# Optimization experiments

Measured on AMD Instinct MI355X. Metric: run time of the kernel, lower is better.

Reference implementation:

```python
import jax, jax.numpy as jnp
import numpy as np
import math

EMBED_DIM = 1024
NUM_HEADS = 16
HEAD_DIM = EMBED_DIM // NUM_HEADS  # 64
MAX_SEQ_LEN = 2048


def rope_tables(max_seq_len, dim):
    pos = jnp.arange(max_seq_len, dtype=jnp.float32)
    div_term = jnp.exp(jnp.arange(0, dim, 2, dtype=jnp.float32) * -(math.log(10000.0) / dim))
    ang = pos[:, None] * div_term[None, :]  # [S, dim//2]
    return jnp.sin(ang), jnp.cos(ang)


def apply_rope(x, sin, cos):
    # x: [B, H, S, D]; sin/cos: [max_seq, D//2]
    S = x.shape[2]
    sin = sin[:S][None, None]  # [1,1,S,D//2]
    cos = cos[:S][None, None]
    x1, x2 = jnp.split(x, 2, axis=-1)
    return jnp.concatenate([cos * x1 - sin * x2, sin * x1 + cos * x2], axis=-1)


def setup_inputs() -> dict:
    key = jax.random.key(0)
    ks = jax.random.split(key, 5)
    B, S, E = 4, 2048, EMBED_DIM
    std = 1.0 / math.sqrt(E)
    x = jax.random.normal(ks[0], (B, S, E), dtype=jnp.float32)
    Wq = jax.random.normal(ks[1], (E, E), dtype=jnp.float32) * std
    Wk = jax.random.normal(ks[2], (E, E), dtype=jnp.float32) * std
    Wv = jax.random.normal(ks[3], (E, E), dtype=jnp.float32) * std
    Wo = jax.random.normal(ks[4], (E, E), dtype=jnp.float32) * std
    return {"x": x, "Wq": Wq, "Wk": Wk, "Wv": Wv, "Wo": Wo}


def reference(x, Wq, Wk, Wv, Wo):
    B, S, E = x.shape
    H, D = NUM_HEADS, HEAD_DIM
    scale = 1.0 / math.sqrt(D)
    sin, cos = rope_tables(MAX_SEQ_LEN, D)

    def split_heads(t):
        return t.reshape(B, S, H, D).transpose(0, 2, 1, 3)  # [B,H,S,D]

    q = split_heads(x @ Wq)
    k = split_heads(x @ Wk)
    v = split_heads(x @ Wv)
    q = apply_rope(q, sin, cos)
    k = apply_rope(k, sin, cos)

    scores = jnp.einsum('bhqd,bhkd->bhqk', q, k) * scale
    causal = jnp.where(jnp.tril(jnp.ones((S, S), dtype=bool)), 0.0, -1e9)
    scores = scores + causal[None, None]
    attn = jax.nn.softmax(scores, axis=-1)
    out = jnp.einsum('bhqk,bhkd->bhqd', attn, v)  # [B,H,S,D]
    out = out.transpose(0, 2, 1, 3).reshape(B, S, E)
    return out @ Wo
```

## Files before the change

kernel.cpp:

```cpp
#include <hip/hip_runtime.h>

#define DEVFN __device__ __forceinline__

typedef __attribute__((ext_vector_type(8))) short bf16x8;
typedef __attribute__((ext_vector_type(4))) float f32x4;
typedef __attribute__((ext_vector_type(16))) float f32x16;

#define MFMA16(a, b, c) __builtin_amdgcn_mfma_f32_16x16x32_bf16(a, b, c, 0, 0, 0)
#define MFMA32(a, b, c) __builtin_amdgcn_mfma_f32_32x32x16_bf16(a, b, c, 0, 0, 0)

DEVFN unsigned short f2bf(float f) {
  union { float f; unsigned u; } v; v.f = f;
  unsigned r = v.u + 0x7FFFu + ((v.u >> 16) & 1u);
  return (unsigned short)(r >> 16);
}
DEVFN unsigned pack2bf(float a, float b) {
  return (unsigned)f2bf(a) | ((unsigned)f2bf(b) << 16);
}
DEVFN unsigned cvtpk(float lo, float hi) {
  unsigned r;
  asm("v_cvt_pk_bf16_f32 %0, %1, %2" : "=v"(r) : "v"(lo), "v"(hi));
  return r;
}
DEVFN void pl32swap(unsigned& a, unsigned& b) {
  asm("v_permlane32_swap_b32 %0, %1" : "+v"(a), "+v"(b));
}
DEVFN void gll16(const void* g, void* l) {
  __builtin_amdgcn_global_load_lds((__attribute__((address_space(1))) void*)g,
                                   (__attribute__((address_space(3))) void*)l,
                                   16, 0, 0);
}


__global__ __launch_bounds__(256) void conv_x_k(const float* __restrict__ x,
                                                unsigned short* __restrict__ xb) {
  int i = (blockIdx.x * 256 + threadIdx.x) * 4;
  float4 v = *(const float4*)(x + i);
  uint2 u;
  u.x = pack2bf(v.x, v.y);
  u.y = pack2bf(v.z, v.w);
  *(uint2*)(xb + i) = u;
}

__global__ __launch_bounds__(256) void transp_k(
    const float* __restrict__ Wq, const float* __restrict__ Wk,
    const float* __restrict__ Wv, const float* __restrict__ Wo,
    unsigned short* __restrict__ Tq, unsigned short* __restrict__ Tk,
    unsigned short* __restrict__ Tv, unsigned short* __restrict__ To) {
  __shared__ unsigned short t[64 * 65];
  int z = blockIdx.z;
  const float* src = (z == 0) ? Wq : (z == 1) ? Wk : (z == 2) ? Wv : Wo;
  unsigned short* dst = (z == 0) ? Tq : (z == 1) ? Tk : (z == 2) ? Tv : To;
  int k0 = blockIdx.x * 64, n0 = blockIdx.y * 64;
  int tid = threadIdx.x;
#pragma unroll
  for (int i = 0; i < 16; ++i) {
    int flat = i * 256 + tid;
    int r = flat >> 6, cc = flat & 63;
    t[cc * 65 + r] = f2bf(src[(size_t)(k0 + r) * 1024 + n0 + cc]);
  }
  __syncthreads();
#pragma unroll
  for (int i = 0; i < 16; ++i) {
    int flat = i * 256 + tid;
    int rr = flat >> 6, cc = flat & 63;
    dst[(size_t)(n0 + rr) * 1024 + k0 + cc] = t[rr * 65 + cc];
  }
}

__global__ __launch_bounds__(256) void rope_k(float* __restrict__ rsin,
                                              float* __restrict__ rcos) {
  int idx = blockIdx.x * 256 + threadIdx.x;
  int s = idx >> 5, j = idx & 31;
  float freq = expf(-0.28782313714981824f * (float)j);
  float ang = (float)s * freq;
  rsin[idx] = sinf(ang);
  rcos[idx] = cosf(ang);
}

template <int MODE>
__global__ __launch_bounds__(256) void gemm_k(
    const unsigned short* __restrict__ A, const unsigned short* __restrict__ WT,
    void* __restrict__ outp, const float* __restrict__ rsin,
    const float* __restrict__ rcos) {
  __shared__ unsigned short At[128 * 64];
  __shared__ unsigned short Bt[128 * 64];
  const int tid = threadIdx.x;
  const int w = tid >> 6, lane = tid & 63, g = lane >> 4, c = lane & 15;
  const int wr = w >> 1, wc = w & 1;
  const int m0 = blockIdx.x * 128, n0 = blockIdx.y * 128;

  f32x4 zero = {0.f, 0.f, 0.f, 0.f};
  f32x4 acc[4][4];
#pragma unroll
  for (int i = 0; i < 4; ++i)
#pragma unroll
    for (int j = 0; j < 4; ++j) acc[i][j] = zero;

  for (int k0 = 0; k0 < 1024; k0 += 64) {
#pragma unroll
    for (int p = 0; p < 4; ++p) {
      int i = p * 256 + tid;
      int row = i >> 3, ls = i & 7;
      size_t off = ((size_t)(m0 + row) * 1024 + k0) * 2 + ((ls ^ (row & 7)) << 4);
      gll16((const char*)A + off, (char*)At + p * 4096 + w * 1024);
      size_t offb = ((size_t)(n0 + row) * 1024 + k0) * 2 + ((ls ^ (row & 7)) << 4);
      gll16((const char*)WT + offb, (char*)Bt + p * 4096 + w * 1024);
    }
    __syncthreads();
#pragma unroll
    for (int ks = 0; ks < 2; ++ks) {
      bf16x8 af[4], bfv[4];
#pragma unroll
      for (int am = 0; am < 4; ++am) {
        int row = wr * 64 + am * 16 + c;
        af[am] = *(const bf16x8*)(At + row * 64 + ((((ks << 2) | g) ^ (row & 7)) << 3));
      }
#pragma unroll
      for (int bn = 0; bn < 4; ++bn) {
        int row = wc * 64 + bn * 16 + c;
        bfv[bn] = *(const bf16x8*)(Bt + row * 64 + ((((ks << 2) | g) ^ (row & 7)) << 3));
      }
#pragma unroll
      for (int am = 0; am < 4; ++am)
#pragma unroll
        for (int bn = 0; bn < 4; ++bn)
          acc[am][bn] = MFMA16(af[am], bfv[bn], acc[am][bn]);
    }
    __syncthreads();
  }

  if (MODE == 0 || MODE == 1) {
    unsigned short* outb = (unsigned short*)outp;
#pragma unroll
    for (int am = 0; am < 4; ++am)
#pragma unroll
      for (int bp = 0; bp < 2; ++bp) {
        int col = n0 + wc * 64 + bp * 16 + c;
        int h = col >> 6, j = col & 63;
#pragma unroll
        for (int r = 0; r < 4; ++r) {
          int row = m0 + wr * 64 + am * 16 + (g << 2) + r;
          int b = row >> 11, s = row & 2047;
          float x1 = acc[am][bp][r], x2 = acc[am][bp + 2][r];
          float sn = rsin[s * 32 + j], cs = rcos[s * 32 + j];
          float o1 = cs * x1 - sn * x2;
          float o2 = sn * x1 + cs * x2;
          if (MODE == 0) {
            o1 *= 0.18033688011112042f;
            o2 *= 0.18033688011112042f;
          }
          size_t base = (((size_t)(b * 16 + h)) * 2048 + s) * 64;
          outb[base + j] = f2bf(o1);
          outb[base + 32 + j] = f2bf(o2);
        }
      }
  } else if (MODE == 2) {
    unsigned short* outb = (unsigned short*)outp;
#pragma unroll
    for (int am = 0; am < 4; ++am)
#pragma unroll
      for (int bn = 0; bn < 4; ++bn) {
        int col = n0 + wc * 64 + bn * 16 + c;
        int h = col >> 6, d = col & 63;
        int row0 = m0 + wr * 64 + am * 16 + (g << 2);
        int b = row0 >> 11, s0 = row0 & 2047;
        uint2 u;
        u.x = pack2bf(acc[am][bn][0], acc[am][bn][1]);
        u.y = pack2bf(acc[am][bn][2], acc[am][bn][3]);
        *(uint2*)(outb + ((size_t)((b * 16 + h) * 64 + d)) * 2048 + s0) = u;
      }
  } else {
    float* outf = (float*)outp;
#pragma unroll
    for (int am = 0; am < 4; ++am)
#pragma unroll
      for (int bn = 0; bn < 4; ++bn)
#pragma unroll
        for (int r = 0; r < 4; ++r)
          outf[(size_t)(m0 + wr * 64 + am * 16 + (g << 2) + r) * 1024 +
               (n0 + wc * 64 + bn * 16 + c)] = acc[am][bn][r];
  }
}

__global__ __launch_bounds__(256, 4) void attn_k(
    const unsigned short* __restrict__ Q, const unsigned short* __restrict__ K,
    const unsigned short* __restrict__ VT, unsigned short* __restrict__ ctx) {
  __shared__ unsigned short Kt[2][64 * 64];
  __shared__ unsigned short Vt[2][64 * 64];

  const int fid = blockIdx.x + (blockIdx.y << 4);
  const int xcd = fid & 7, j = fid >> 3;
  const int bh = (xcd << 3) + (j >> 4);
  const int p = j & 15;
  const int qtB = 31 - p;

  const int tid = threadIdx.x;
  const int w = tid >> 6, lane = tid & 63;
  const int hi = lane >> 5, c5 = lane & 31;
  const int myIsB = ((w >> 1) == (fid & 1));
  const int myTile = myIsB ? qtB : p;
  const int myLast = myTile;
  const int qw = myTile * 64 + (w & 1) * 32;

  const unsigned short* Qbh = Q + (size_t)bh * 2048 * 64;
  const unsigned short* Kbh = K + (size_t)bh * 2048 * 64;
  const unsigned short* VTbh = VT + (size_t)bh * 64 * 2048;

  bf16x8 qf[4];
#pragma unroll
  for (int kb = 0; kb < 4; ++kb)
    qf[kb] = *(const bf16x8*)(Qbh + (size_t)(qw + c5) * 64 + kb * 16 + hi * 8);

  f32x16 oacc[2];
#pragma unroll
  for (int dt = 0; dt < 2; ++dt)
#pragma unroll
    for (int i = 0; i < 16; ++i) oacc[dt][i] = 0.f;
  float m_run = -1e30f, l_run = 0.f;

  auto stage = [&](int st, int buf) {
    const int kv0 = st * 64;
#pragma unroll
    for (int pp = 0; pp < 2; ++pp) {
      int i = pp * 256 + tid;
      int row = i >> 3, ls = i & 7;
      gll16((const char*)Kbh + (size_t)(kv0 + row) * 128 + ((ls ^ (row & 7)) << 4),
            (char*)(&Kt[buf][0]) + pp * 4096 + w * 1024);
      gll16((const char*)VTbh + (size_t)row * 4096 + (size_t)kv0 * 2 +
                ((ls ^ (row & 7)) << 4),
            (char*)(&Vt[buf][0]) + pp * 4096 + w * 1024);
    }
  };

  stage(0, 0);
  __syncthreads();

  for (int st = 0; st <= qtB; ++st) {
    const int cur = st & 1;
    if (st < qtB) stage(st + 1, cur ^ 1);

    if (st <= myLast) {
      const unsigned short* Kb_ = &Kt[cur][0];
      const unsigned short* Vb_ = &Vt[cur][0];

      f32x16 sacc[2];
#pragma unroll
      for (int t = 0; t < 2; ++t)
#pragma unroll
        for (int i = 0; i < 16; ++i) sacc[t][i] = 0.f;
#pragma unroll
      for (int t = 0; t < 2; ++t) {
        const int row = t * 32 + c5;
#pragma unroll
        for (int kb = 0; kb < 4; ++kb) {
          bf16x8 kf = *(const bf16x8*)(Kb_ + row * 64 +
                                       (((2 * kb + hi) ^ (c5 & 7)) << 3));
          sacc[t] = MFMA32(kf, qf[kb], sacc[t]);
        }
      }

      if (st == myLast) {
        const int q = qw + c5;
#pragma unroll
        for (int t = 0; t < 2; ++t) {
          const int kvb = st * 64 + t * 32 + (hi << 2);
#pragma unroll
          for (int i = 0; i < 16; ++i) {
            int kv = kvb + (i & 3) + ((i >> 2) << 3);
            if (kv > q) sacc[t][i] = -1e30f;
          }
        }
      }

      float vmax = -1e30f;
#pragma unroll
      for (int t = 0; t < 2; ++t)
#pragma unroll
        for (int i = 0; i < 16; ++i) vmax = fmaxf(vmax, sacc[t][i]);
      vmax = fmaxf(vmax, __shfl_xor(vmax, 32, 64));
      if (!__all(vmax <= m_run + 8.0f)) {
        float m_new = fmaxf(m_run, vmax);
        float alpha = exp2f(m_run - m_new);
        l_run *= alpha;
#pragma unroll
        for (int dt = 0; dt < 2; ++dt)
#pragma unroll
          for (int i = 0; i < 16; ++i) oacc[dt][i] *= alpha;
        m_run = m_new;
      }
      float psum = 0.f;
#pragma unroll
      for (int t = 0; t < 2; ++t)
#pragma unroll
        for (int i = 0; i < 16; ++i) {
          float pv = exp2f(sacc[t][i] - m_run);
          sacc[t][i] = pv;
          psum += pv;
        }
      psum += __shfl_xor(psum, 32, 64);
      l_run += psum;

      unsigned pword[4][4];
#pragma unroll
      for (int t = 0; t < 2; ++t) {
        unsigned X[4][2];
#pragma unroll
        for (int u = 0; u < 4; ++u)
#pragma unroll
          for (int wp = 0; wp < 2; ++wp)
            X[u][wp] = cvtpk(sacc[t][u * 4 + 2 * wp], sacc[t][u * 4 + 2 * wp + 1]);
#pragma unroll
        for (int par = 0; par < 2; ++par) {
          const int kb = 2 * t + par;
#pragma unroll
          for (int wp = 0; wp < 2; ++wp) {
            unsigned a = X[2 * par][wp], b2 = X[2 * par + 1][wp];
            pl32swap(a, b2);
            pword[kb][wp] = a;
            pword[kb][wp + 2] = b2;
          }
        }
      }

#pragma unroll
      for (int kb = 0; kb < 4; ++kb) {
        union { unsigned u[4]; bf16x8 v; } pw;
#pragma unroll
        for (int k2 = 0; k2 < 4; ++k2) pw.u[k2] = pword[kb][k2];
#pragma unroll
        for (int dt = 0; dt < 2; ++dt) {
          const int row = dt * 32 + c5;
          bf16x8 vf = *(const bf16x8*)(Vb_ + row * 64 +
                                       (((2 * kb + hi) ^ (c5 & 7)) << 3));
          oacc[dt] = MFMA32(vf, pw.v, oacc[dt]);
        }
      }
    }
    __syncthreads();
  }

  const int b = bh >> 4, h = bh & 15;
  const float linv = 1.f / l_run;
  unsigned short* crow = ctx + ((size_t)(b * 2048 + qw + c5)) * 1024 + h * 64;
#pragma unroll
  for (int dt = 0; dt < 2; ++dt)
#pragma unroll
    for (int u = 0; u < 4; ++u) {
      int d0 = dt * 32 + 8 * u + 4 * hi;
      uint2 o;
      o.x = cvtpk(oacc[dt][4 * u] * linv, oacc[dt][4 * u + 1] * linv);
      o.y = cvtpk(oacc[dt][4 * u + 2] * linv, oacc[dt][4 * u + 3] * linv);
      *(uint2*)(crow + d0) = o;
    }
}


extern "C" void kernel_launch(void* const* d_in, const int* in_sizes, int n_in,
                              void* d_out, int out_size, void* d_ws, size_t ws_size,
                              hipStream_t stream) {
  (void)in_sizes; (void)n_in; (void)out_size; (void)ws_size;
  const float* x = (const float*)d_in[0];
  const float* Wq = (const float*)d_in[1];
  const float* Wk = (const float*)d_in[2];
  const float* Wv = (const float*)d_in[3];
  const float* Wo = (const float*)d_in[4];
  char* ws = (char*)d_ws;
  const size_t MiB = 1024 * 1024;
  unsigned short* xb  = (unsigned short*)(ws);
  unsigned short* WTq = (unsigned short*)(ws + 16 * MiB);
  unsigned short* WTk = (unsigned short*)(ws + 18 * MiB);
  unsigned short* WTv = (unsigned short*)(ws + 20 * MiB);
  unsigned short* WTo = (unsigned short*)(ws + 22 * MiB);
  unsigned short* Qb  = (unsigned short*)(ws + 24 * MiB);
  unsigned short* Kb  = (unsigned short*)(ws + 40 * MiB);
  unsigned short* VTb = (unsigned short*)(ws + 56 * MiB);
  unsigned short* ctx = (unsigned short*)(ws + 72 * MiB);
  float* rsin = (float*)(ws + 88 * MiB);
  float* rcos = (float*)(ws + 88 * MiB + 256 * 1024);

  conv_x_k<<<8192, 256, 0, stream>>>(x, xb);
  transp_k<<<dim3(16, 16, 4), 256, 0, stream>>>(Wq, Wk, Wv, Wo, WTq, WTk, WTv, WTo);
  rope_k<<<256, 256, 0, stream>>>(rsin, rcos);
  gemm_k<0><<<dim3(64, 8), 256, 0, stream>>>(xb, WTq, Qb, rsin, rcos);
  gemm_k<1><<<dim3(64, 8), 256, 0, stream>>>(xb, WTk, Kb, rsin, rcos);
  gemm_k<2><<<dim3(64, 8), 256, 0, stream>>>(xb, WTv, VTb, rsin, rcos);
  attn_k<<<dim3(16, 64), 256, 0, stream>>>(Qb, Kb, VTb, ctx);
  gemm_k<3><<<dim3(64, 8), 256, 0, stream>>>(ctx, WTo, d_out, rsin, rcos);
}
```

Measured before the change: 199.0 us.

## Restructure attention LDS layout, compute row sums via MFMA, interleave rope tables

The K/V tiles in LDS now use a chunk-major layout (8 chunks of 64 rows x 16 bytes) in place of the XOR-swizzled row layout. This simplifies the address math for the global-to-LDS loads and the LDS reads. The softmax row sum is now taken from an extra MFMA against a ones vector rather than a scalar add and cross-lane shuffle. The MFMA sections gain s_setprio hints, and the max reduction is paired. The RoPE sin/cos tables are interleaved into float2 so the GEMM epilogue does one load instead of two. The extra MFMA per kv block adds matrix work and 16 accumulator registers, which may affect occupancy.

```diff
diff --git a/kernel.cpp b/kernel.cpp
--- a/kernel.cpp
+++ b/kernel.cpp
@@ -68,21 +68,18 @@
   }
 }
 
-__global__ __launch_bounds__(256) void rope_k(float* __restrict__ rsin,
-                                              float* __restrict__ rcos) {
+__global__ __launch_bounds__(256) void rope_k(float2* __restrict__ rtab) {
   int idx = blockIdx.x * 256 + threadIdx.x;
   int s = idx >> 5, j = idx & 31;
   float freq = expf(-0.28782313714981824f * (float)j);
   float ang = (float)s * freq;
-  rsin[idx] = sinf(ang);
-  rcos[idx] = cosf(ang);
+  rtab[idx] = make_float2(sinf(ang), cosf(ang));
 }
 
 template <int MODE>
 __global__ __launch_bounds__(256) void gemm_k(
     const unsigned short* __restrict__ A, const unsigned short* __restrict__ WT,
-    void* __restrict__ outp, const float* __restrict__ rsin,
-    const float* __restrict__ rcos) {
+    void* __restrict__ outp, const float2* __restrict__ rtab) {
   __shared__ unsigned short At[128 * 64];
   __shared__ unsigned short Bt[128 * 64];
   const int tid = threadIdx.x;
@@ -143,9 +140,9 @@
           int row = m0 + wr * 64 + am * 16 + (g << 2) + r;
           int b = row >> 11, s = row & 2047;
           float x1 = acc[am][bp][r], x2 = acc[am][bp + 2][r];
-          float sn = rsin[s * 32 + j], cs = rcos[s * 32 + j];
-          float o1 = cs * x1 - sn * x2;
-          float o2 = sn * x1 + cs * x2;
+          float2 sc = rtab[s * 32 + j];
+          float o1 = sc.y * x1 - sc.x * x2;
+          float o2 = sc.x * x1 + sc.y * x2;
           if (MODE == 0) {
             o1 *= 0.18033688011112042f;
             o2 *= 0.18033688011112042f;
@@ -186,8 +183,8 @@
 __global__ __launch_bounds__(256, 4) void attn_k(
     const unsigned short* __restrict__ Q, const unsigned short* __restrict__ K,
     const unsigned short* __restrict__ VT, unsigned short* __restrict__ ctx) {
-  __shared__ unsigned short Kt[2][64 * 64];
-  __shared__ unsigned short Vt[2][64 * 64];
+  __shared__ unsigned short Kt[2][8 * 64 * 8];
+  __shared__ unsigned short Vt[2][8 * 64 * 8];
 
   const int fid = blockIdx.x + (blockIdx.y << 4);
   const int xcd = fid & 7, j = fid >> 3;
@@ -212,24 +209,25 @@
   for (int kb = 0; kb < 4; ++kb)
     qf[kb] = *(const bf16x8*)(Qbh + (size_t)(qw + c5) * 64 + kb * 16 + hi * 8);
 
-  f32x16 oacc[2];
-#pragma unroll
-  for (int dt = 0; dt < 2; ++dt)
-#pragma unroll
-    for (int i = 0; i < 16; ++i) oacc[dt][i] = 0.f;
-  float m_run = -1e30f, l_run = 0.f;
+  bf16x8 ones;
+#pragma unroll
+  for (int i = 0; i < 8; ++i) ones[i] = (short)0x3F80;
+
+  f32x16 zacc;
+#pragma unroll
+  for (int i = 0; i < 16; ++i) zacc[i] = 0.f;
+  f32x16 oacc[2], lacc;
+  oacc[0] = zacc; oacc[1] = zacc; lacc = zacc;
+  float m_run = -1e30f;
 
   auto stage = [&](int st, int buf) {
-    const int kv0 = st * 64;
+    const char* ksrc = (const char*)Kbh + (size_t)(st * 64 + lane) * 128;
+    const char* vsrc = (const char*)VTbh + (size_t)lane * 4096 + (size_t)st * 128;
 #pragma unroll
     for (int pp = 0; pp < 2; ++pp) {
-      int i = pp * 256 + tid;
-      int row = i >> 3, ls = i & 7;
-      gll16((const char*)Kbh + (size_t)(kv0 + row) * 128 + ((ls ^ (row & 7)) << 4),
-            (char*)(&Kt[buf][0]) + pp * 4096 + w * 1024);
-      gll16((const char*)VTbh + (size_t)row * 4096 + (size_t)kv0 * 2 +
-                ((ls ^ (row & 7)) << 4),
-            (char*)(&Vt[buf][0]) + pp * 4096 + w * 1024);
+      const int m = pp * 4 + w;
+      gll16(ksrc + m * 16, (char*)(&Kt[buf][0]) + m * 1024);
+      gll16(vsrc + m * 16, (char*)(&Vt[buf][0]) + m * 1024);
     }
   };
 
@@ -245,20 +243,19 @@
       const unsigned short* Vb_ = &Vt[cur][0];
 
       f32x16 sacc[2];
-#pragma unroll
-      for (int t = 0; t < 2; ++t)
-#pragma unroll
-        for (int i = 0; i < 16; ++i) sacc[t][i] = 0.f;
+      __builtin_amdgcn_s_setprio(1);
 #pragma unroll
       for (int t = 0; t < 2; ++t) {
-        const int row = t * 32 + c5;
-#pragma unroll
-        for (int kb = 0; kb < 4; ++kb) {
-          bf16x8 kf = *(const bf16x8*)(Kb_ + row * 64 +
-                                       (((2 * kb + hi) ^ (c5 & 7)) << 3));
+        const int ro = (t * 32 + c5) * 8;
+        bf16x8 kf0 = *(const bf16x8*)(Kb_ + hi * 512 + ro);
+        sacc[t] = MFMA32(kf0, qf[0], zacc);
+#pragma unroll
+        for (int kb = 1; kb < 4; ++kb) {
+          bf16x8 kf = *(const bf16x8*)(Kb_ + (2 * kb + hi) * 512 + ro);
           sacc[t] = MFMA32(kf, qf[kb], sacc[t]);
         }
       }
+      __builtin_amdgcn_s_setprio(0);
 
       if (st == myLast) {
         const int q = qw + c5;
@@ -273,33 +270,28 @@
         }
       }
 
-      float vmax = -1e30f;
+      float vmax = fmaxf(sacc[0][0], sacc[0][1]);
 #pragma unroll
       for (int t = 0; t < 2; ++t)
 #pragma unroll
-        for (int i = 0; i < 16; ++i) vmax = fmaxf(vmax, sacc[t][i]);
+        for (int i = (t == 0 ? 2 : 0); i < 16; i += 2)
+          vmax = fmaxf(vmax, fmaxf(sacc[t][i], sacc[t][i + 1]));
       vmax = fmaxf(vmax, __shfl_xor(vmax, 32, 64));
       if (!__all(vmax <= m_run + 8.0f)) {
         float m_new = fmaxf(m_run, vmax);
         float alpha = exp2f(m_run - m_new);
-        l_run *= alpha;
-#pragma unroll
-        for (int dt = 0; dt < 2; ++dt)
-#pragma unroll
-          for (int i = 0; i < 16; ++i) oacc[dt][i] *= alpha;
+#pragma unroll
+        for (int i = 0; i < 16; ++i) {
+          oacc[0][i] *= alpha;
+          oacc[1][i] *= alpha;
+          lacc[i] *= alpha;
+        }
         m_run = m_new;
       }
-      float psum = 0.f;
 #pragma unroll
       for (int t = 0; t < 2; ++t)
 #pragma unroll
-        for (int i = 0; i < 16; ++i) {
-          float pv = exp2f(sacc[t][i] - m_run);
-          sacc[t][i] = pv;
-          psum += pv;
-        }
-      psum += __shfl_xor(psum, 32, 64);
-      l_run += psum;
+        for (int i = 0; i < 16; ++i) sacc[t][i] = exp2f(sacc[t][i] - m_run);
 
       unsigned pword[4][4];
 #pragma unroll
@@ -323,25 +315,27 @@
         }
       }
 
+      __builtin_amdgcn_s_setprio(1);
 #pragma unroll
       for (int kb = 0; kb < 4; ++kb) {
         union { unsigned u[4]; bf16x8 v; } pw;
 #pragma unroll
         for (int k2 = 0; k2 < 4; ++k2) pw.u[k2] = pword[kb][k2];
+        const int so = (2 * kb + hi) * 512;
 #pragma unroll
         for (int dt = 0; dt < 2; ++dt) {
-          const int row = dt * 32 + c5;
-          bf16x8 vf = *(const bf16x8*)(Vb_ + row * 64 +
-                                       (((2 * kb + hi) ^ (c5 & 7)) << 3));
+          bf16x8 vf = *(const bf16x8*)(Vb_ + so + (dt * 32 + c5) * 8);
           oacc[dt] = MFMA32(vf, pw.v, oacc[dt]);
         }
-      }
+        lacc = MFMA32(ones, pw.v, lacc);
+      }
+      __builtin_amdgcn_s_setprio(0);
     }
     __syncthreads();
   }
 
   const int b = bh >> 4, h = bh & 15;
-  const float linv = 1.f / l_run;
+  const float linv = 1.f / lacc[0];
   unsigned short* crow = ctx + ((size_t)(b * 2048 + qw + c5)) * 1024 + h * 64;
 #pragma unroll
   for (int dt = 0; dt < 2; ++dt)
@@ -376,15 +370,14 @@
   unsigned short* Kb  = (unsigned short*)(ws + 40 * MiB);
   unsigned short* VTb = (unsigned short*)(ws + 56 * MiB);
   unsigned short* ctx = (unsigned short*)(ws + 72 * MiB);
-  float* rsin = (float*)(ws + 88 * MiB);
-  float* rcos = (float*)(ws + 88 * MiB + 256 * 1024);
+  float2* rtab = (float2*)(ws + 88 * MiB);
 
   conv_x_k<<<8192, 256, 0, stream>>>(x, xb);
   transp_k<<<dim3(16, 16, 4), 256, 0, stream>>>(Wq, Wk, Wv, Wo, WTq, WTk, WTv, WTo);
-  rope_k<<<256, 256, 0, stream>>>(rsin, rcos);
-  gemm_k<0><<<dim3(64, 8), 256, 0, stream>>>(xb, WTq, Qb, rsin, rcos);
-  gemm_k<1><<<dim3(64, 8), 256, 0, stream>>>(xb, WTk, Kb, rsin, rcos);
-  gemm_k<2><<<dim3(64, 8), 256, 0, stream>>>(xb, WTv, VTb, rsin, rcos);
+  rope_k<<<256, 256, 0, stream>>>(rtab);
+  gemm_k<0><<<dim3(64, 8), 256, 0, stream>>>(xb, WTq, Qb, rtab);
+  gemm_k<1><<<dim3(64, 8), 256, 0, stream>>>(xb, WTk, Kb, rtab);
+  gemm_k<2><<<dim3(64, 8), 256, 0, stream>>>(xb, WTv, VTb, rtab);
   attn_k<<<dim3(16, 64), 256, 0, stream>>>(Qb, Kb, VTb, ctx);
-  gemm_k<3><<<dim3(64, 8), 256, 0, stream>>>(ctx, WTo, d_out, rsin, rcos);
-}
+  gemm_k<3><<<dim3(64, 8), 256, 0, stream>>>(ctx, WTo, d_out, rtab);
+}
```

Result: slower. 203.6 us (+2.3%).
